# Performance work log

Measured on AMD Instinct MI355X. Metric: run time of the kernel, lower is better.

The kernel has to match this reference:

```python
import jax, jax.numpy as jnp
import numpy as np

N = 45056      # 2048 instances * 22 machines
E = 720896     # avg degree 16
FEA = 60       # max_num*6
HID = 256
MACH = 22
NEG_SLOPE = 0.01


def setup_inputs() -> dict:
    key = jax.random.key(0)
    ks = jax.random.split(key, 20)
    x = jax.random.normal(ks[0], (N, FEA), dtype=jnp.float32)
    edge_index = jax.random.randint(ks[1], (2, E), 0, N, dtype=jnp.int64)
    edge_weight = jax.random.uniform(ks[2], (E,), dtype=jnp.float32)

    def lin(k, fan_in, fan_out):
        s = 1.0 / np.sqrt(fan_in)
        kw, kb = jax.random.split(k)
        W = jax.random.uniform(kw, (fan_in, fan_out), minval=-s, maxval=s, dtype=jnp.float32)
        b = jax.random.uniform(kb, (fan_out,), minval=-s, maxval=s, dtype=jnp.float32)
        return W, b

    W1, b1 = lin(ks[3], FEA, HID)
    W2, b2 = lin(ks[4], HID, HID)
    mlp_in = MACH * (HID + FEA)  # 6952
    Wf0, bf0 = lin(ks[5], mlp_in, HID)
    Wf1, bf1 = lin(ks[6], HID, HID)
    Wf2, bf2 = lin(ks[7], HID, HID)
    Wo, bo = lin(ks[8], HID, 4)
    return {"x": x, "edge_index": edge_index, "edge_weight": edge_weight,
            "W1": W1, "b1": b1, "W2": W2, "b2": b2,
            "Wf0": Wf0, "bf0": bf0, "Wf1": Wf1, "bf1": bf1,
            "Wf2": Wf2, "bf2": bf2, "Wo": Wo, "bo": bo}


def _gcn_conv(h, W, b, row, col, norm, n):
    # h' = scatter_add(norm * (hW)[row] -> col) + b   (PyG GCNConv)
    hw = h @ W                                  # [N, out]
    msg = hw[row] * norm[:, None]               # [E+N, out]
    out = jax.ops.segment_sum(msg, col, num_segments=n)
    return out + b


def reference(x, edge_index, edge_weight, W1, b1, W2, b2,
              Wf0, bf0, Wf1, bf1, Wf2, bf2, Wo, bo):
    n = x.shape[0]
    # gcn_norm with self-loops (fill_value=1.0), symmetric normalization
    loop = jnp.arange(n, dtype=edge_index.dtype)
    row = jnp.concatenate([edge_index[0], loop])
    col = jnp.concatenate([edge_index[1], loop])
    ew = jnp.concatenate([edge_weight, jnp.ones((n,), dtype=edge_weight.dtype)])
    deg = jax.ops.segment_sum(ew, col, num_segments=n)
    dinv = jnp.where(deg > 0, jax.lax.rsqrt(jnp.maximum(deg, 1e-12)), 0.0)
    norm = dinv[row] * ew * dinv[col]

    h = _gcn_conv(x, W1, b1, row, col, norm, n)
    h = jax.nn.leaky_relu(h, NEG_SLOPE)
    # dropout p=0.5 is identity in eval mode
    h = _gcn_conv(h, W2, b2, row, col, norm, n)
    h = jax.nn.leaky_relu(h, NEG_SLOPE)

    h = jnp.concatenate([h, x], axis=1)         # [N, HID+FEA]
    flat = h.reshape(n // MACH, -1)             # [B, 22*(HID+FEA)]

    z = jax.nn.leaky_relu(flat @ Wf0 + bf0, NEG_SLOPE)
    z = jax.nn.leaky_relu(z @ Wf1 + bf1, NEG_SLOPE)
    z = jax.nn.leaky_relu(z @ Wf2 + bf2, NEG_SLOPE)
    return z @ Wo + bo                           # [B, 4]
```

## Files before the change

kernel.cpp:

```cpp
#include <hip/hip_runtime.h>
#include <stdint.h>

#define FEA 60
#define HID 256
#define MACH 22
#define PERM 316
#define PERM2 320
#define FLATP2 (MACH * PERM2)
#define NEG 0.01f
#define BCAP 64
#define S0 16
#define KC0 448

typedef __bf16 bf16x8 __attribute__((ext_vector_type(8)));
typedef float f32x4 __attribute__((ext_vector_type(4)));

__device__ __forceinline__ float bf2f(uint16_t u) {
    return __uint_as_float(((uint32_t)u) << 16);
}
__device__ __forceinline__ uint16_t f2bf(float f) {
    uint32_t x = __float_as_uint(f);
    return (uint16_t)((x + 0x7fffu + ((x >> 16) & 1u)) >> 16);
}

__global__ void k_detect_init(const uint32_t* ew_w, const uint32_t* ei_w, int* flags,
                              int* count, float* z0acc, int n) {
    int i = blockIdx.x * blockDim.x + threadIdx.x;
    if (i < n) count[i] = 0;
    z0acc[i] = 0.f;
    if (blockIdx.x == 0) {
        __shared__ int c15, onz;
        if (threadIdx.x == 0) { c15 = 0; onz = 0; }
        __syncthreads();
        int a = 0, b = 0;
        for (int k = threadIdx.x; k < 1024; k += 256) {
            if (ew_w[k] & 0x8000u) a++;
            if (ei_w[2 * k + 1] != 0u) b++;
        }
        atomicAdd(&c15, a); atomicAdd(&onz, b);
        __syncthreads();
        if (threadIdx.x == 0) {
            flags[0] = (c15 <= 100) ? 1 : 0;
            flags[1] = (onz < 8) ? 1 : 0;
        }
    }
}

struct PrepAll {
    const void* xsrc; uint16_t* x64;
    const void* src8[8]; float* dst8[8]; long prefix[9]; int cnt8;
    const void* wf0; uint16_t* wf0t;
    const void* src3[3]; uint16_t* dst3[3];
    const void* w1; uint16_t* w1t;
    const void* ei; const void* ew; int* count; uint2* adj; int E;
    int n;
};

#define NB_CVT 1024
#define NB_TR  492

__global__ __launch_bounds__(256) void k_prep_all(PrepAll a, const int* flags) {
    int isbf = flags[0];
    int b = blockIdx.x;
    int t = threadIdx.x;
    if (b < NB_CVT) {
        long nx = (long)a.n * 64;
        long total = nx + a.prefix[a.cnt8];
        for (long i = (long)b * 256 + t; i < total; i += (long)NB_CVT * 256) {
            if (i < nx) {
                int col = (int)(i & 63);
                long row = i >> 6;
                uint16_t v = 0;
                if (col < FEA) {
                    long s = row * FEA + col;
                    v = isbf ? ((const uint16_t*)a.xsrc)[s] : f2bf(((const float*)a.xsrc)[s]);
                }
                a.x64[i] = v;
            } else {
                long ii = i - nx;
                int tt = 0;
                while (ii >= a.prefix[tt + 1]) tt++;
                long j = ii - a.prefix[tt];
                a.dst8[tt][j] = isbf ? bf2f(((const uint16_t*)a.src8[tt])[j])
                                     : ((const float*)a.src8[tt])[j];
            }
        }
    } else if (b < NB_CVT + NB_TR) {
        __shared__ uint16_t s[64][65];
        int bb = b - NB_CVT;
        if (bb < 440) {
            int g0 = (bb >> 2) * 64, n0 = (bb & 3) * 64;
#pragma unroll
            for (int i = 0; i < 16; i++) {
                int idx = t + i * 256;
                int gg = idx >> 6, nn = idx & 63;
                int gk = g0 + gg;
                int m = gk / PERM2;
                int k2 = gk - m * PERM2;
                uint16_t v = 0;
                if (k2 < PERM) {
                    long off = (long)(m * PERM + k2) * HID + n0 + nn;
                    v = isbf ? ((const uint16_t*)a.wf0)[off] : f2bf(((const float*)a.wf0)[off]);
                }
                s[gg][nn] = v;
            }
            __syncthreads();
#pragma unroll
            for (int i = 0; i < 16; i++) {
                int idx = t + i * 256;
                int nn = idx >> 6, gg = idx & 63;
                a.wf0t[(long)(n0 + nn) * FLATP2 + g0 + gg] = s[gg][nn];
            }
        } else if (bb < 488) {
            int idx0 = bb - 440;
            int z = idx0 >> 4, r = idx0 & 15;
            int k0 = (r >> 2) * 64, n0 = (r & 3) * 64;
            const void* W = a.src3[z];
            uint16_t* Wt = a.dst3[z];
#pragma unroll
            for (int i = 0; i < 16; i++) {
                int idx = t + i * 256;
                int kk = idx >> 6, nn = idx & 63;
                long off = (long)(k0 + kk) * HID + n0 + nn;
                s[kk][nn] = isbf ? ((const uint16_t*)W)[off] : f2bf(((const float*)W)[off]);
            }
            __syncthreads();
#pragma unroll
            for (int i = 0; i < 16; i++) {
                int idx = t + i * 256;
                int nn = idx >> 6, kk = idx & 63;
                Wt[(long)(n0 + nn) * HID + k0 + kk] = s[kk][nn];
            }
        } else {
            int n0 = (bb - 488) * 64;
#pragma unroll
            for (int i = 0; i < 16; i++) {
                int idx = t + i * 256;
                int kk = idx >> 6, nn = idx & 63;
                uint16_t v = 0;
                if (kk < FEA) {
                    long off = (long)kk * HID + n0 + nn;
                    v = isbf ? ((const uint16_t*)a.w1)[off] : f2bf(((const float*)a.w1)[off]);
                }
                s[kk][nn] = v;
            }
            __syncthreads();
#pragma unroll
            for (int i = 0; i < 16; i++) {
                int idx = t + i * 256;
                int nn = idx >> 6, kk = idx & 63;
                a.w1t[(long)(n0 + nn) * 64 + kk] = s[kk][nn];
            }
        }
    } else {
        int e0 = ((b - NB_CVT - NB_TR) * 256 + t) * 2;
        int E = a.E;
        if (e0 >= E) return;
        int i64 = flags[1];
        int r0, r1 = -1, c0, c1 = -1;
        if (i64) {
            const long long* pr = (const long long*)a.ei + e0;
            const long long* pc = (const long long*)a.ei + E + e0;
            r0 = (int)pr[0]; c0 = (int)pc[0];
            if (e0 + 1 < E) { r1 = (int)pr[1]; c1 = (int)pc[1]; }
        } else {
            const int* pr = (const int*)a.ei + e0;
            const int* pc = (const int*)a.ei + E + e0;
            r0 = pr[0]; c0 = pc[0];
            if (e0 + 1 < E) { r1 = pr[1]; c1 = pc[1]; }
        }
        float w0, w1 = 0.f;
        if (isbf) {
            uint32_t ww = ((const uint32_t*)a.ew)[e0 >> 1];
            w0 = bf2f((uint16_t)(ww & 0xffff));
            w1 = bf2f((uint16_t)(ww >> 16));
        } else {
            float2 f = ((const float2*)a.ew)[e0 >> 1];
            w0 = f.x; w1 = f.y;
        }
        int p0 = atomicAdd(&a.count[c0], 1);
        uint2 v0; v0.x = (uint32_t)r0; v0.y = __float_as_uint(w0);
        a.adj[((long)c0 << 6) + p0] = v0;
        if (c1 >= 0) {
            int p1 = atomicAdd(&a.count[c1], 1);
            uint2 v1; v1.x = (uint32_t)r1; v1.y = __float_as_uint(w1);
            a.adj[((long)c1 << 6) + p1] = v1;
        }
    }
}

__global__ void k_rowsum(const int* count, const uint2* adj, float* dinv, int n) {
    int i = blockIdx.x * blockDim.x + threadIdx.x;
    if (i >= n) return;
    int cnt = count[i];
    const uint2* row = adj + ((long)i << 6);
    double d = 1.0;
    for (int p = 0; p < cnt; p++) d += (double)__uint_as_float(row[p].y);
    dinv[i] = (float)(1.0 / sqrt(d));
}

__global__ __launch_bounds__(256) void k_aggx(const uint16_t* __restrict__ x64,
                                              const float* __restrict__ dinv,
                                              const int* __restrict__ count,
                                              const uint2* __restrict__ adj,
                                              uint16_t* __restrict__ xa, int n) {
    __shared__ uint2 sadj[8][32];
    int hv = threadIdx.x >> 5;
    int l = threadIdx.x & 31;
    int node = blockIdx.x * 8 + hv;
    if (node >= n) return;
    const uint32_t* xu = (const uint32_t*)x64;
    float di = dinv[node];
    float c2 = di * di;
    uint32_t h = xu[(long)node * 32 + l];
    float a0 = c2 * bf2f((uint16_t)(h & 0xffff));
    float a1 = c2 * bf2f((uint16_t)(h >> 16));
    int cnt = count[node];
    const uint2* row = adj + ((long)node << 6);
    for (int base = 0; base < cnt; base += 32) {
        int m = cnt - base; if (m > 32) m = 32;
        if (l < m) {
            uint2 a = row[base + l];
            float w = __uint_as_float(a.y) * dinv[a.x] * di;
            uint2 p; p.x = a.x; p.y = __float_as_uint(w);
            sadj[hv][l] = p;
        }
        int t = 0;
        for (; t + 4 <= m; t += 4) {
            uint2 e0 = sadj[hv][t], e1 = sadj[hv][t + 1], e2 = sadj[hv][t + 2], e3 = sadj[hv][t + 3];
            uint32_t v0 = xu[(long)e0.x * 32 + l];
            uint32_t v1 = xu[(long)e1.x * 32 + l];
            uint32_t v2 = xu[(long)e2.x * 32 + l];
            uint32_t v3 = xu[(long)e3.x * 32 + l];
            float w0 = __uint_as_float(e0.y), w1 = __uint_as_float(e1.y);
            float w2 = __uint_as_float(e2.y), w3 = __uint_as_float(e3.y);
            a0 += w0 * bf2f((uint16_t)(v0 & 0xffff)); a1 += w0 * bf2f((uint16_t)(v0 >> 16));
            a0 += w1 * bf2f((uint16_t)(v1 & 0xffff)); a1 += w1 * bf2f((uint16_t)(v1 >> 16));
            a0 += w2 * bf2f((uint16_t)(v2 & 0xffff)); a1 += w2 * bf2f((uint16_t)(v2 >> 16));
            a0 += w3 * bf2f((uint16_t)(v3 & 0xffff)); a1 += w3 * bf2f((uint16_t)(v3 >> 16));
        }
        for (; t < m; t++) {
            uint2 e0 = sadj[hv][t];
            uint32_t v0 = xu[(long)e0.x * 32 + l];
            float w0 = __uint_as_float(e0.y);
            a0 += w0 * bf2f((uint16_t)(v0 & 0xffff));
            a1 += w0 * bf2f((uint16_t)(v0 >> 16));
        }
    }
    ((uint32_t*)xa)[(long)node * 32 + l] =
        (uint32_t)f2bf(a0) | ((uint32_t)f2bf(a1) << 16);
}

__device__ __forceinline__ void fma8(float* acc, float w, uint4 v) {
    acc[0] += w * bf2f((uint16_t)(v.x & 0xffff));
    acc[1] += w * bf2f((uint16_t)(v.x >> 16));
    acc[2] += w * bf2f((uint16_t)(v.y & 0xffff));
    acc[3] += w * bf2f((uint16_t)(v.y >> 16));
    acc[4] += w * bf2f((uint16_t)(v.z & 0xffff));
    acc[5] += w * bf2f((uint16_t)(v.z >> 16));
    acc[6] += w * bf2f((uint16_t)(v.w & 0xffff));
    acc[7] += w * bf2f((uint16_t)(v.w >> 16));
}

__global__ __launch_bounds__(256) void k_aggb(const uint16_t* __restrict__ hw,
                                              const float* __restrict__ dinv,
                                              const int* __restrict__ count,
                                              const uint2* __restrict__ adj,
                                              const float* __restrict__ bias,
                                              uint16_t* __restrict__ out, int n) {
    __shared__ uint2 sadj[8][32];
    int hv = threadIdx.x >> 5;
    int l = threadIdx.x & 31;
    int node = blockIdx.x * 8 + hv;
    if (node >= n) return;
    const uint4* hw4 = (const uint4*)hw;
    float di = dinv[node];
    float c2 = di * di;
    uint4 h = hw4[(long)node * 32 + l];
    float acc[8];
    acc[0] = c2 * bf2f((uint16_t)(h.x & 0xffff));
    acc[1] = c2 * bf2f((uint16_t)(h.x >> 16));
    acc[2] = c2 * bf2f((uint16_t)(h.y & 0xffff));
    acc[3] = c2 * bf2f((uint16_t)(h.y >> 16));
    acc[4] = c2 * bf2f((uint16_t)(h.z & 0xffff));
    acc[5] = c2 * bf2f((uint16_t)(h.z >> 16));
    acc[6] = c2 * bf2f((uint16_t)(h.w & 0xffff));
    acc[7] = c2 * bf2f((uint16_t)(h.w >> 16));
    int cnt = count[node];
    const uint2* row = adj + ((long)node << 6);
    for (int base = 0; base < cnt; base += 32) {
        int m = cnt - base; if (m > 32) m = 32;
        if (l < m) {
            uint2 a = row[base + l];
            float w = __uint_as_float(a.y) * dinv[a.x] * di;
            uint2 p; p.x = a.x; p.y = __float_as_uint(w);
            sadj[hv][l] = p;
        }
        int t = 0;
        for (; t + 4 <= m; t += 4) {
            uint2 e0 = sadj[hv][t], e1 = sadj[hv][t + 1], e2 = sadj[hv][t + 2], e3 = sadj[hv][t + 3];
            uint4 v0 = hw4[(long)e0.x * 32 + l];
            uint4 v1 = hw4[(long)e1.x * 32 + l];
            uint4 v2 = hw4[(long)e2.x * 32 + l];
            uint4 v3 = hw4[(long)e3.x * 32 + l];
            fma8(acc, __uint_as_float(e0.y), v0);
            fma8(acc, __uint_as_float(e1.y), v1);
            fma8(acc, __uint_as_float(e2.y), v2);
            fma8(acc, __uint_as_float(e3.y), v3);
        }
        for (; t < m; t++) {
            uint2 e0 = sadj[hv][t];
            uint4 v0 = hw4[(long)e0.x * 32 + l];
            fma8(acc, __uint_as_float(e0.y), v0);
        }
    }
    float4 ba = ((const float4*)bias)[l * 2];
    float4 bb = ((const float4*)bias)[l * 2 + 1];
    acc[0] += ba.x; acc[1] += ba.y; acc[2] += ba.z; acc[3] += ba.w;
    acc[4] += bb.x; acc[5] += bb.y; acc[6] += bb.z; acc[7] += bb.w;
#pragma unroll
    for (int k = 0; k < 8; k++) acc[k] = acc[k] > 0.f ? acc[k] : NEG * acc[k];
    uint4 o;
    o.x = (uint32_t)f2bf(acc[0]) | ((uint32_t)f2bf(acc[1]) << 16);
    o.y = (uint32_t)f2bf(acc[2]) | ((uint32_t)f2bf(acc[3]) << 16);
    o.z = (uint32_t)f2bf(acc[4]) | ((uint32_t)f2bf(acc[5]) << 16);
    o.w = (uint32_t)f2bf(acc[6]) | ((uint32_t)f2bf(acc[7]) << 16);
    ((uint4*)out)[(long)node * 32 + l] = o;
}

__global__ __launch_bounds__(256) void k_mgemm(const uint16_t* __restrict__ A,
                                               const uint16_t* __restrict__ Bt,
                                               uint16_t* __restrict__ outb,
                                               const float* __restrict__ bias,
                                               int M, int K, int act) {
    __shared__ uint16_t As[128 * 40];
    __shared__ uint16_t Bs[128 * 40];
    int tid = threadIdx.x;
    int lane = tid & 63, wv = tid >> 6;
    int quad = lane >> 4, l15 = lane & 15;
    int row0 = blockIdx.y * 128, col0 = blockIdx.x * 128;
    int arow = (wv >> 1) * 64;
    int bcol = (wv & 1) * 64;

    f32x4 acc[4][4];
#pragma unroll
    for (int i = 0; i < 4; i++)
#pragma unroll
        for (int j = 0; j < 4; j++) acc[i][j] = (f32x4){0.f, 0.f, 0.f, 0.f};

    for (int kc = 0; kc < K; kc += 32) {
#pragma unroll
        for (int i = 0; i < 2; i++) {
            int idx = tid + i * 256;
            int r = idx >> 2, cq = idx & 3;
            uint4 va = *(const uint4*)(A + (long)(row0 + r) * K + kc + cq * 8);
            *(uint4*)(&As[r * 40 + cq * 8]) = va;
            uint4 vb = *(const uint4*)(Bt + (long)(col0 + r) * K + kc + cq * 8);
            *(uint4*)(&Bs[r * 40 + cq * 8]) = vb;
        }
        __syncthreads();
        bf16x8 af[4], bfr[4];
#pragma unroll
        for (int i = 0; i < 4; i++)
            af[i] = __builtin_bit_cast(bf16x8,
                *(const uint4*)(&As[(arow + i * 16 + l15) * 40 + quad * 8]));
#pragma unroll
        for (int j = 0; j < 4; j++)
            bfr[j] = __builtin_bit_cast(bf16x8,
                *(const uint4*)(&Bs[(bcol + j * 16 + l15) * 40 + quad * 8]));
#pragma unroll
        for (int i = 0; i < 4; i++)
#pragma unroll
            for (int j = 0; j < 4; j++)
                acc[i][j] = __builtin_amdgcn_mfma_f32_16x16x32_bf16(af[i], bfr[j], acc[i][j], 0, 0, 0);
        __syncthreads();
    }

#pragma unroll
    for (int i = 0; i < 4; i++)
#pragma unroll
        for (int j = 0; j < 4; j++) {
            int row = row0 + arow + i * 16 + quad * 4;
            int col = col0 + bcol + j * 16 + l15;
#pragma unroll
            for (int reg = 0; reg < 4; reg++) {
                float v = acc[i][j][reg];
                if (bias) v += bias[col];
                if (act) v = v > 0.f ? v : NEG * v;
                outb[(long)(row + reg) * HID + col] = f2bf(v);
            }
        }
}

__global__ __launch_bounds__(256) void k_mgemm_flat(const uint16_t* __restrict__ h2,
                                                    const uint16_t* __restrict__ x64,
                                                    const uint16_t* __restrict__ Bt,
                                                    float* __restrict__ z0acc,
                                                    int M) {
    __shared__ uint16_t As[128 * 40];
    __shared__ uint16_t Bs[128 * 40];
    int tid = threadIdx.x;
    int lane = tid & 63, wv = tid >> 6;
    int quad = lane >> 4, l15 = lane & 15;
    int row0 = blockIdx.y * 128, col0 = blockIdx.x * 128;
    int kbeg = blockIdx.z * KC0;
    int kend = kbeg + KC0; if (kend > FLATP2) kend = FLATP2;
    int arow = (wv >> 1) * 64;
    int bcol = (wv & 1) * 64;

    f32x4 acc[4][4];
#pragma unroll
    for (int i = 0; i < 4; i++)
#pragma unroll
        for (int j = 0; j < 4; j++) acc[i][j] = (f32x4){0.f, 0.f, 0.f, 0.f};

    for (int kc = kbeg; kc < kend; kc += 32) {
#pragma unroll
        for (int i = 0; i < 2; i++) {
            int idx = tid + i * 256;
            int r = idx >> 2, cq = idx & 3;
            int gk = kc + cq * 8;
            int m = gk / PERM2;
            int k2 = gk - m * PERM2;
            long node = (long)(row0 + r) * MACH + m;
            uint4 va = (k2 < HID)
                ? *(const uint4*)(h2 + node * HID + k2)
                : *(const uint4*)(x64 + node * 64 + (k2 - HID));
            *(uint4*)(&As[r * 40 + cq * 8]) = va;
            uint4 vb = *(const uint4*)(Bt + (long)(col0 + r) * FLATP2 + gk);
            *(uint4*)(&Bs[r * 40 + cq * 8]) = vb;
        }
        __syncthreads();
        bf16x8 af[4], bfr[4];
#pragma unroll
        for (int i = 0; i < 4; i++)
            af[i] = __builtin_bit_cast(bf16x8,
                *(const uint4*)(&As[(arow + i * 16 + l15) * 40 + quad * 8]));
#pragma unroll
        for (int j = 0; j < 4; j++)
            bfr[j] = __builtin_bit_cast(bf16x8,
                *(const uint4*)(&Bs[(bcol + j * 16 + l15) * 40 + quad * 8]));
#pragma unroll
        for (int i = 0; i < 4; i++)
#pragma unroll
            for (int j = 0; j < 4; j++)
                acc[i][j] = __builtin_amdgcn_mfma_f32_16x16x32_bf16(af[i], bfr[j], acc[i][j], 0, 0, 0);
        __syncthreads();
    }

#pragma unroll
    for (int i = 0; i < 4; i++)
#pragma unroll
        for (int j = 0; j < 4; j++) {
            int row = row0 + arow + i * 16 + quad * 4;
            int col = col0 + bcol + j * 16 + l15;
#pragma unroll
            for (int reg = 0; reg < 4; reg++)
                atomicAdd(&z0acc[(long)(row + reg) * HID + col], acc[i][j][reg]);
        }
}

__global__ __launch_bounds__(256) void k_tail(const float* __restrict__ z0acc,
                                              const float* __restrict__ bf0,
                                              const uint16_t* __restrict__ Wf1t,
                                              const float* __restrict__ bf1,
                                              const uint16_t* __restrict__ Wf2t,
                                              const float* __restrict__ bf2,
                                              const float* __restrict__ Wo,
                                              const float* __restrict__ bo,
                                              void* out, const int* flags) {
    __shared__ uint16_t z0s[16 * 256];
    __shared__ uint16_t z1s[16 * 256];
    __shared__ uint16_t z2s[16 * 256];
    int tid = threadIdx.x;
    int lane = tid & 63, wv = tid >> 6;
    int quad = lane >> 4, l15 = lane & 15;
    int rows0 = blockIdx.x * 16;
    int nw = wv * 64;

    for (int i = tid; i < 16 * 256; i += 256) {
        int rr = i >> 8, cc = i & 255;
        float v = z0acc[(long)(rows0 + rr) * HID + cc] + bf0[cc];
        v = v > 0.f ? v : NEG * v;
        z0s[i] = f2bf(v);
    }
    __syncthreads();

    {
        f32x4 acc[4];
#pragma unroll
        for (int j = 0; j < 4; j++) acc[j] = (f32x4){0.f, 0.f, 0.f, 0.f};
        for (int kc = 0; kc < HID; kc += 32) {
            bf16x8 a = __builtin_bit_cast(bf16x8,
                *(const uint4*)(&z0s[l15 * 256 + kc + quad * 8]));
#pragma unroll
            for (int j = 0; j < 4; j++) {
                bf16x8 b = __builtin_bit_cast(bf16x8,
                    *(const uint4*)(Wf1t + (long)(nw + j * 16 + l15) * HID + kc + quad * 8));
                acc[j] = __builtin_amdgcn_mfma_f32_16x16x32_bf16(a, b, acc[j], 0, 0, 0);
            }
        }
#pragma unroll
        for (int j = 0; j < 4; j++) {
            int col = nw + j * 16 + l15;
            float bj = bf1[col];
#pragma unroll
            for (int reg = 0; reg < 4; reg++) {
                float v = acc[j][reg] + bj;
                v = v > 0.f ? v : NEG * v;
                z1s[(quad * 4 + reg) * 256 + col] = f2bf(v);
            }
        }
    }
    __syncthreads();

    {
        f32x4 acc[4];
#pragma unroll
        for (int j = 0; j < 4; j++) acc[j] = (f32x4){0.f, 0.f, 0.f, 0.f};
        for (int kc = 0; kc < HID; kc += 32) {
            bf16x8 a = __builtin_bit_cast(bf16x8,
                *(const uint4*)(&z1s[l15 * 256 + kc + quad * 8]));
#pragma unroll
            for (int j = 0; j < 4; j++) {
                bf16x8 b = __builtin_bit_cast(bf16x8,
                    *(const uint4*)(Wf2t + (long)(nw + j * 16 + l15) * HID + kc + quad * 8));
                acc[j] = __builtin_amdgcn_mfma_f32_16x16x32_bf16(a, b, acc[j], 0, 0, 0);
            }
        }
#pragma unroll
        for (int j = 0; j < 4; j++) {
            int col = nw + j * 16 + l15;
            float bj = bf2[col];
#pragma unroll
            for (int reg = 0; reg < 4; reg++) {
                float v = acc[j][reg] + bj;
                v = v > 0.f ? v : NEG * v;
                z2s[(quad * 4 + reg) * 256 + col] = f2bf(v);
            }
        }
    }
    __syncthreads();

    if (tid < 64) {
        int r = tid >> 2, o = tid & 3;
        float acc = bo[o];
        for (int k = 0; k < HID; k++)
            acc += bf2f(z2s[r * 256 + k]) * Wo[k * 4 + o];
        long idx = (long)(rows0 + r) * 4 + o;
        if (flags[0]) ((uint16_t*)out)[idx] = f2bf(acc);
        else          ((float*)out)[idx] = acc;
    }
}

extern "C" void kernel_launch(void* const* d_in, const int* in_sizes, int n_in,
                              void* d_out, int out_size, void* d_ws, size_t ws_size,
                              hipStream_t stream) {
    const int N  = in_sizes[0] / FEA;
    const int E  = in_sizes[2];
    const int Bn = N / MACH;

    char* ws = (char*)d_ws;
    size_t off = 0;
    auto alloc = [&](size_t bytes) -> char* {
        char* p = ws + off;
        off = (off + bytes + 255) & ~(size_t)255;
        return p;
    };

    int*      flags  = (int*)     alloc(64);
    uint16_t* x64    = (uint16_t*)alloc((size_t)N * 64 * 2);
    uint16_t* xa     = (uint16_t*)alloc((size_t)N * 64 * 2);
    uint16_t* W1t    = (uint16_t*)alloc((size_t)HID * 64 * 2);
    uint16_t* W2t    = (uint16_t*)alloc((size_t)HID * HID * 2);
    uint16_t* Wf0t   = (uint16_t*)alloc((size_t)HID * FLATP2 * 2);
    uint16_t* Wf1t   = (uint16_t*)alloc((size_t)HID * HID * 2);
    uint16_t* Wf2t   = (uint16_t*)alloc((size_t)HID * HID * 2);
    float*    b1     = (float*)   alloc(HID * 4);
    float*    b2     = (float*)   alloc(HID * 4);
    float*    bf0    = (float*)   alloc(HID * 4);
    float*    bf1    = (float*)   alloc(HID * 4);
    float*    bf2    = (float*)   alloc(HID * 4);
    float*    Wo     = (float*)   alloc((size_t)HID * 4 * 4);
    float*    bo     = (float*)   alloc(4 * 4);
    int*      count  = (int*)     alloc((size_t)N * 4);
    uint2*    adj    = (uint2*)   alloc((size_t)N * BCAP * 8);
    float*    dinv   = (float*)   alloc((size_t)N * 4);
    uint16_t* P      = (uint16_t*)alloc((size_t)N * HID * 2);
    uint16_t* Q      = (uint16_t*)alloc((size_t)N * HID * 2);
    float*    z0acc  = (float*)   alloc((size_t)Bn * HID * 4);
    (void)ws_size; (void)n_in; (void)out_size;

    k_detect_init<<<(Bn * HID) / 256, 256, 0, stream>>>(
        (const uint32_t*)d_in[2], (const uint32_t*)d_in[1], flags, count, z0acc, N);

    PrepAll pa{};
    pa.xsrc = d_in[0]; pa.x64 = x64;
    const void* s8[7] = { d_in[4], d_in[6], d_in[8], d_in[10], d_in[12], d_in[13], d_in[14] };
    float* d8[7] = { b1, b2, bf0, bf1, bf2, Wo, bo };
    long n8[7] = { HID, HID, HID, HID, HID, (long)HID * 4, 4 };
    pa.cnt8 = 7;
    pa.prefix[0] = 0;
    for (int t = 0; t < 7; t++) { pa.src8[t] = s8[t]; pa.dst8[t] = d8[t]; pa.prefix[t + 1] = pa.prefix[t] + n8[t]; }
    pa.prefix[8] = pa.prefix[7];
    pa.wf0 = d_in[7]; pa.wf0t = Wf0t;
    pa.src3[0] = d_in[5];  pa.dst3[0] = W2t;
    pa.src3[1] = d_in[9];  pa.dst3[1] = Wf1t;
    pa.src3[2] = d_in[11]; pa.dst3[2] = Wf2t;
    pa.w1 = d_in[3]; pa.w1t = W1t;
    pa.ei = d_in[1]; pa.ew = d_in[2]; pa.count = count; pa.adj = adj; pa.E = E;
    pa.n = N;
    int nb_sc = (E / 2 + 255) / 256;
    k_prep_all<<<NB_CVT + NB_TR + nb_sc, 256, 0, stream>>>(pa, flags);

    k_rowsum<<<(N + 255) / 256, 256, 0, stream>>>(count, adj, dinv, N);

    k_aggx<<<(N + 7) / 8, 256, 0, stream>>>(x64, dinv, count, adj, xa, N);
    k_mgemm<<<dim3(2, N / 128), 256, 0, stream>>>(xa, W1t, P, b1, N, 64, 1);

    k_mgemm<<<dim3(2, N / 128), 256, 0, stream>>>(P, W2t, Q, nullptr, N, HID, 0);
    k_aggb<<<(N + 7) / 8, 256, 0, stream>>>(Q, dinv, count, adj, b2, P, N);

    k_mgemm_flat<<<dim3(2, Bn / 128, S0), 256, 0, stream>>>(P, x64, Wf0t, z0acc, Bn);

    k_tail<<<Bn / 16, 256, 0, stream>>>(z0acc, bf0, Wf1t, bf1, Wf2t, bf2, Wo, bo,
                                        d_out, flags);
}
```

Before: 317.2 us.

## Split GCN aggregation across column-group blocks and use nontemporal adjacency stores

The aggregation kernels now assign 16 lanes per node and split the feature columns across blocks (2 groups for the input aggregation, 8 for the hidden one). Each thread handles one bf16 pair instead of eight, which raises parallelism and shrinks per-thread register use. The cost is that each node's adjacency list is reloaded and its weights recomputed once per column group. Adjacency writes in the scatter kernel become 64-bit nontemporal stores so they do not pollute the cache.

```diff
diff --git a/kernel.cpp b/kernel.cpp
--- a/kernel.cpp
+++ b/kernel.cpp
@@ -179,12 +179,14 @@
             w0 = f.x; w1 = f.y;
         }
         int p0 = atomicAdd(&a.count[c0], 1);
-        uint2 v0; v0.x = (uint32_t)r0; v0.y = __float_as_uint(w0);
-        a.adj[((long)c0 << 6) + p0] = v0;
+        unsigned long long v0 = (unsigned long long)(uint32_t)r0 |
+                                ((unsigned long long)__float_as_uint(w0) << 32);
+        __builtin_nontemporal_store(v0, (unsigned long long*)&a.adj[((long)c0 << 6) + p0]);
         if (c1 >= 0) {
             int p1 = atomicAdd(&a.count[c1], 1);
-            uint2 v1; v1.x = (uint32_t)r1; v1.y = __float_as_uint(w1);
-            a.adj[((long)c1 << 6) + p1] = v1;
+            unsigned long long v1 = (unsigned long long)(uint32_t)r1 |
+                                    ((unsigned long long)__float_as_uint(w1) << 32);
+            __builtin_nontemporal_store(v1, (unsigned long long*)&a.adj[((long)c1 << 6) + p1]);
         }
     }
 }
@@ -204,34 +206,38 @@
                                               const int* __restrict__ count,
                                               const uint2* __restrict__ adj,
                                               uint16_t* __restrict__ xa, int n) {
-    __shared__ uint2 sadj[8][32];
-    int hv = threadIdx.x >> 5;
-    int l = threadIdx.x & 31;
-    int node = blockIdx.x * 8 + hv;
+    __shared__ uint2 sadj[16][16];
+    int cg = blockIdx.x & 1;
+    int ng = blockIdx.x >> 1;
+    int slot = threadIdx.x >> 4;
+    int l = threadIdx.x & 15;
+    int node = ng * 16 + slot;
     if (node >= n) return;
     const uint32_t* xu = (const uint32_t*)x64;
+    int cbase = cg * 16;
     float di = dinv[node];
     float c2 = di * di;
-    uint32_t h = xu[(long)node * 32 + l];
+    uint32_t h = xu[(long)node * 32 + cbase + l];
     float a0 = c2 * bf2f((uint16_t)(h & 0xffff));
     float a1 = c2 * bf2f((uint16_t)(h >> 16));
     int cnt = count[node];
     const uint2* row = adj + ((long)node << 6);
-    for (int base = 0; base < cnt; base += 32) {
-        int m = cnt - base; if (m > 32) m = 32;
+    for (int base = 0; base < cnt; base += 16) {
+        int m = cnt - base; if (m > 16) m = 16;
         if (l < m) {
             uint2 a = row[base + l];
             float w = __uint_as_float(a.y) * dinv[a.x] * di;
             uint2 p; p.x = a.x; p.y = __float_as_uint(w);
-            sadj[hv][l] = p;
+            sadj[slot][l] = p;
         }
         int t = 0;
         for (; t + 4 <= m; t += 4) {
-            uint2 e0 = sadj[hv][t], e1 = sadj[hv][t + 1], e2 = sadj[hv][t + 2], e3 = sadj[hv][t + 3];
-            uint32_t v0 = xu[(long)e0.x * 32 + l];
-            uint32_t v1 = xu[(long)e1.x * 32 + l];
-            uint32_t v2 = xu[(long)e2.x * 32 + l];
-            uint32_t v3 = xu[(long)e3.x * 32 + l];
+            uint2 e0 = sadj[slot][t], e1 = sadj[slot][t + 1];
+            uint2 e2 = sadj[slot][t + 2], e3 = sadj[slot][t + 3];
+            uint32_t v0 = xu[(long)e0.x * 32 + cbase + l];
+            uint32_t v1 = xu[(long)e1.x * 32 + cbase + l];
+            uint32_t v2 = xu[(long)e2.x * 32 + cbase + l];
+            uint32_t v3 = xu[(long)e3.x * 32 + cbase + l];
             float w0 = __uint_as_float(e0.y), w1 = __uint_as_float(e1.y);
             float w2 = __uint_as_float(e2.y), w3 = __uint_as_float(e3.y);
             a0 += w0 * bf2f((uint16_t)(v0 & 0xffff)); a1 += w0 * bf2f((uint16_t)(v0 >> 16));
@@ -240,26 +246,15 @@
             a0 += w3 * bf2f((uint16_t)(v3 & 0xffff)); a1 += w3 * bf2f((uint16_t)(v3 >> 16));
         }
         for (; t < m; t++) {
-            uint2 e0 = sadj[hv][t];
-            uint32_t v0 = xu[(long)e0.x * 32 + l];
+            uint2 e0 = sadj[slot][t];
+            uint32_t v0 = xu[(long)e0.x * 32 + cbase + l];
             float w0 = __uint_as_float(e0.y);
             a0 += w0 * bf2f((uint16_t)(v0 & 0xffff));
             a1 += w0 * bf2f((uint16_t)(v0 >> 16));
         }
     }
-    ((uint32_t*)xa)[(long)node * 32 + l] =
+    ((uint32_t*)xa)[(long)node * 32 + cbase + l] =
         (uint32_t)f2bf(a0) | ((uint32_t)f2bf(a1) << 16);
-}
-
-__device__ __forceinline__ void fma8(float* acc, float w, uint4 v) {
-    acc[0] += w * bf2f((uint16_t)(v.x & 0xffff));
-    acc[1] += w * bf2f((uint16_t)(v.x >> 16));
-    acc[2] += w * bf2f((uint16_t)(v.y & 0xffff));
-    acc[3] += w * bf2f((uint16_t)(v.y >> 16));
-    acc[4] += w * bf2f((uint16_t)(v.z & 0xffff));
-    acc[5] += w * bf2f((uint16_t)(v.z >> 16));
-    acc[6] += w * bf2f((uint16_t)(v.w & 0xffff));
-    acc[7] += w * bf2f((uint16_t)(v.w >> 16));
 }
 
 __global__ __launch_bounds__(256) void k_aggb(const uint16_t* __restrict__ hw,
@@ -268,64 +263,59 @@
                                               const uint2* __restrict__ adj,
                                               const float* __restrict__ bias,
                                               uint16_t* __restrict__ out, int n) {
-    __shared__ uint2 sadj[8][32];
-    int hv = threadIdx.x >> 5;
-    int l = threadIdx.x & 31;
-    int node = blockIdx.x * 8 + hv;
+    __shared__ uint2 sadj[16][16];
+    int cg = blockIdx.x & 7;
+    int ng = blockIdx.x >> 3;
+    int slot = threadIdx.x >> 4;
+    int l = threadIdx.x & 15;
+    int node = ng * 16 + slot;
     if (node >= n) return;
-    const uint4* hw4 = (const uint4*)hw;
+    const uint32_t* hwu = (const uint32_t*)hw;
+    int cbase = cg * 16;
     float di = dinv[node];
     float c2 = di * di;
-    uint4 h = hw4[(long)node * 32 + l];
-    float acc[8];
-    acc[0] = c2 * bf2f((uint16_t)(h.x & 0xffff));
-    acc[1] = c2 * bf2f((uint16_t)(h.x >> 16));
-    acc[2] = c2 * bf2f((uint16_t)(h.y & 0xffff));
-    acc[3] = c2 * bf2f((uint16_t)(h.y >> 16));
-    acc[4] = c2 * bf2f((uint16_t)(h.z & 0xffff));
-    acc[5] = c2 * bf2f((uint16_t)(h.z >> 16));
-    acc[6] = c2 * bf2f((uint16_t)(h.w & 0xffff));
-    acc[7] = c2 * bf2f((uint16_t)(h.w >> 16));
+    uint32_t h = hwu[(long)node * 128 + cbase + l];
+    float a0 = c2 * bf2f((uint16_t)(h & 0xffff));
+    float a1 = c2 * bf2f((uint16_t)(h >> 16));
     int cnt = count[node];
     const uint2* row = adj + ((long)node << 6);
-    for (int base = 0; base < cnt; base += 32) {
-        int m = cnt - base; if (m > 32) m = 32;
+    for (int base = 0; base < cnt; base += 16) {
+        int m = cnt - base; if (m > 16) m = 16;
         if (l < m) {
             uint2 a = row[base + l];
             float w = __uint_as_float(a.y) * dinv[a.x] * di;
             uint2 p; p.x = a.x; p.y = __float_as_uint(w);
-            sadj[hv][l] = p;
+            sadj[slot][l] = p;
         }
         int t = 0;
         for (; t + 4 <= m; t += 4) {
-            uint2 e0 = sadj[hv][t], e1 = sadj[hv][t + 1], e2 = sadj[hv][t + 2], e3 = sadj[hv][t + 3];
-            uint4 v0 = hw4[(long)e0.x * 32 + l];
-            uint4 v1 = hw4[(long)e1.x * 32 + l];
-            uint4 v2 = hw4[(long)e2.x * 32 + l];
-            uint4 v3 = hw4[(long)e3.x * 32 + l];
-            fma8(acc, __uint_as_float(e0.y), v0);
-            fma8(acc, __uint_as_float(e1.y), v1);
-            fma8(acc, __uint_as_float(e2.y), v2);
-            fma8(acc, __uint_as_float(e3.y), v3);
+            uint2 e0 = sadj[slot][t], e1 = sadj[slot][t + 1];
+            uint2 e2 = sadj[slot][t + 2], e3 = sadj[slot][t + 3];
+            uint32_t v0 = hwu[(long)e0.x * 128 + cbase + l];
+            uint32_t v1 = hwu[(long)e1.x * 128 + cbase + l];
+            uint32_t v2 = hwu[(long)e2.x * 128 + cbase + l];
+            uint32_t v3 = hwu[(long)e3.x * 128 + cbase + l];
+            float w0 = __uint_as_float(e0.y), w1 = __uint_as_float(e1.y);
+            float w2 = __uint_as_float(e2.y), w3 = __uint_as_float(e3.y);
+            a0 += w0 * bf2f((uint16_t)(v0 & 0xffff)); a1 += w0 * bf2f((uint16_t)(v0 >> 16));
+            a0 += w1 * bf2f((uint16_t)(v1 & 0xffff)); a1 += w1 * bf2f((uint16_t)(v1 >> 16));
+            a0 += w2 * bf2f((uint16_t)(v2 & 0xffff)); a1 += w2 * bf2f((uint16_t)(v2 >> 16));
+            a0 += w3 * bf2f((uint16_t)(v3 & 0xffff)); a1 += w3 * bf2f((uint16_t)(v3 >> 16));
         }
         for (; t < m; t++) {
-            uint2 e0 = sadj[hv][t];
-            uint4 v0 = hw4[(long)e0.x * 32 + l];
-            fma8(acc, __uint_as_float(e0.y), v0);
-        }
-    }
-    float4 ba = ((const float4*)bias)[l * 2];
-    float4 bb = ((const float4*)bias)[l * 2 + 1];
-    acc[0] += ba.x; acc[1] += ba.y; acc[2] += ba.z; acc[3] += ba.w;
-    acc[4] += bb.x; acc[5] += bb.y; acc[6] += bb.z; acc[7] += bb.w;
-#pragma unroll
-    for (int k = 0; k < 8; k++) acc[k] = acc[k] > 0.f ? acc[k] : NEG * acc[k];
-    uint4 o;
-    o.x = (uint32_t)f2bf(acc[0]) | ((uint32_t)f2bf(acc[1]) << 16);
-    o.y = (uint32_t)f2bf(acc[2]) | ((uint32_t)f2bf(acc[3]) << 16);
-    o.z = (uint32_t)f2bf(acc[4]) | ((uint32_t)f2bf(acc[5]) << 16);
-    o.w = (uint32_t)f2bf(acc[6]) | ((uint32_t)f2bf(acc[7]) << 16);
-    ((uint4*)out)[(long)node * 32 + l] = o;
+            uint2 e0 = sadj[slot][t];
+            uint32_t v0 = hwu[(long)e0.x * 128 + cbase + l];
+            float w0 = __uint_as_float(e0.y);
+            a0 += w0 * bf2f((uint16_t)(v0 & 0xffff));
+            a1 += w0 * bf2f((uint16_t)(v0 >> 16));
+        }
+    }
+    float2 bv = ((const float2*)bias)[cbase + l];
+    a0 += bv.x; a1 += bv.y;
+    a0 = a0 > 0.f ? a0 : NEG * a0;
+    a1 = a1 > 0.f ? a1 : NEG * a1;
+    ((uint32_t*)out)[(long)node * 128 + cbase + l] =
+        (uint32_t)f2bf(a0) | ((uint32_t)f2bf(a1) << 16);
 }
 
 __global__ __launch_bounds__(256) void k_mgemm(const uint16_t* __restrict__ A,
@@ -615,11 +605,11 @@
 
     k_rowsum<<<(N + 255) / 256, 256, 0, stream>>>(count, adj, dinv, N);
 
-    k_aggx<<<(N + 7) / 8, 256, 0, stream>>>(x64, dinv, count, adj, xa, N);
+    k_aggx<<<2 * ((N + 15) / 16), 256, 0, stream>>>(x64, dinv, count, adj, xa, N);
     k_mgemm<<<dim3(2, N / 128), 256, 0, stream>>>(xa, W1t, P, b1, N, 64, 1);
 
     k_mgemm<<<dim3(2, N / 128), 256, 0, stream>>>(P, W2t, Q, nullptr, N, HID, 0);
-    k_aggb<<<(N + 7) / 8, 256, 0, stream>>>(Q, dinv, count, adj, b2, P, N);
+    k_aggb<<<8 * ((N + 15) / 16), 256, 0, stream>>>(Q, dinv, count, adj, b2, P, N);
 
     k_mgemm_flat<<<dim3(2, Bn / 128, S0), 256, 0, stream>>>(P, x64, Wf0t, z0acc, Bn);
 
```

Result: slower. 370.5 us (+16.8%).
